# Kernel tuning notes

Hardware: AMD Instinct MI355X
Metric: run time of the kernel (lower is better)

The kernel has to match this reference:

```python
import jax, jax.numpy as jnp
import numpy as np

B, S, HID = 1, 2048, 2048
H, D, R = 16, 256, 64          # heads, head_dim, qk_rope_head_dim
NOPE = D - R
QL, OR, G = 1024, 512, 4       # q_lora_rank, o_lora_rank, o_groups
HPG = H // G
EPS = 1e-6
SCALE = D ** -0.5
STD = 0.02


def setup_inputs() -> dict:
    key = jax.random.key(0)
    ks = jax.random.split(key, 9)
    return {
        "x": jax.random.normal(ks[0], (B, S, HID), jnp.float32),
        "freqs": jax.random.uniform(ks[1], (B, S, R // 2), jnp.float32) * 6.2831853,
        "wq_a": jax.random.normal(ks[2], (QL, HID), jnp.float32) * STD,
        "q_norm_w": jnp.ones((QL,), jnp.float32),
        "wq_b": jax.random.normal(ks[3], (H * D, QL), jnp.float32) * STD,
        "wkv": jax.random.normal(ks[4], (D, HID), jnp.float32) * STD,
        "kv_norm_w": jnp.ones((D,), jnp.float32),
        "wo_a_w": jax.random.normal(ks[5], (G * OR, HPG * D), jnp.float32) * STD,
        "wo_b": jax.random.normal(ks[6], (HID, G * OR), jnp.float32) * STD,
        "attn_sink": jnp.zeros((H,), jnp.float32),
    }


def _rms(x, w):
    return x * jax.lax.rsqrt(jnp.mean(jnp.square(x), -1, keepdims=True) + EPS) * w


def _rot(t, cos, sin, conj=False):
    # t: [..., R]; cos/sin broadcastable to [..., R//2]
    tr = t.reshape(*t.shape[:-1], R // 2, 2)
    x1, x2 = tr[..., 0], tr[..., 1]
    if conj:
        sin = -sin
    out = jnp.stack([x1 * cos - x2 * sin, x1 * sin + x2 * cos], axis=-1)
    return out.reshape(t.shape)


def reference(x, freqs, wq_a, q_norm_w, wq_b, wkv, kv_norm_w, wo_a_w, wo_b, attn_sink):
    cos = jnp.cos(freqs)  # [B,S,R/2]
    sin = jnp.sin(freqs)

    # Q path: LoRA down -> RMSNorm -> up, then per-head RMS rescale (no weight)
    q = _rms(x @ wq_a.T, q_norm_w) @ wq_b.T          # [B,S,H*D]
    q = q.reshape(B, S, H, D)
    q = q * jax.lax.rsqrt(jnp.mean(jnp.square(q), -1, keepdims=True) + EPS)
    q_nope, q_pe = q[..., :NOPE], q[..., NOPE:]

    # shared latent K=V
    kv = _rms(x @ wkv.T, kv_norm_w)                  # [B,S,D]
    kv_nope, kv_pe = kv[..., :NOPE], kv[..., NOPE:]

    # partial RoPE
    q_pe = _rot(q_pe, cos[:, :, None, :], sin[:, :, None, :])
    kv_pe = _rot(kv_pe, cos, sin)

    q = jnp.concatenate([q_nope, q_pe], -1)          # [B,S,H,D]
    kv = jnp.concatenate([kv_nope, kv_pe], -1)       # [B,S,D] shared across heads

    # attention with causal mask + per-head sink column
    scores = jnp.einsum("bshd,btd->bhst", q, kv) * SCALE   # [B,H,S,S]
    mask = jnp.tril(jnp.ones((S, S), bool))
    scores = jnp.where(mask, scores, -jnp.inf)
    sink = jnp.broadcast_to(attn_sink[None, :, None, None], (B, H, S, 1))
    probs = jax.nn.softmax(jnp.concatenate([scores, sink], -1), axis=-1)[..., :-1]
    o = jnp.einsum("bhst,btd->bshd", probs, kv)      # [B,S,H,D]

    # un-rotate the rope part of the output (multiply by conj(freqs_cis))
    o_nope, o_pe = o[..., :NOPE], o[..., NOPE:]
    o_pe = _rot(o_pe, cos[:, :, None, :], sin[:, :, None, :], conj=True)
    o = jnp.concatenate([o_nope, o_pe], -1)

    # grouped (block-diagonal) output LoRA, then up-projection
    o_g = o.reshape(B, S, G, HPG * D)
    w = wo_a_w.reshape(G, OR, HPG * D)
    o_r = jnp.einsum("bsgd,grd->bsgr", o_g, w).reshape(B, S, G * OR)
    return o_r @ wo_b.T                              # [B,S,HID]
```

## Files before the change

kernel.cpp:

```cpp
#include <hip/hip_runtime.h>
#include <hip/hip_bf16.h>

#define S_LEN 2048
#define HID 2048
#define NH 16
#define HD 256
#define NROT 64
#define NOPE 192
#define QL 1024
#define OR_ 512
#define NG 4
#define HPG 4
#define EPS 1e-6f
#define SCALE 0.0625f

typedef __bf16 bf16x8 __attribute__((ext_vector_type(8)));
typedef short s16x8 __attribute__((ext_vector_type(8)));
typedef float f32x4 __attribute__((ext_vector_type(4)));

#define MFMA(a, b, c) __builtin_amdgcn_mfma_f32_16x16x32_bf16( \
    __builtin_bit_cast(bf16x8, a), __builtin_bit_cast(bf16x8, b), c, 0, 0, 0)

__device__ __forceinline__ unsigned short f2bf(float x) {
  unsigned int u = __builtin_bit_cast(unsigned int, x);
  u += 0x7FFFu + ((u >> 16) & 1u);
  return (unsigned short)(u >> 16);
}
__device__ __forceinline__ float bf2f(unsigned short b) {
  unsigned int u = ((unsigned int)b) << 16;
  return __builtin_bit_cast(float, u);
}

#define GLD_LDS16(gp, lp) __builtin_amdgcn_global_load_lds( \
    (__attribute__((address_space(1))) void*)(gp), \
    (__attribute__((address_space(3))) void*)(lp), 16, 0, 0)

__global__ __launch_bounds__(256) void f32_to_bf16(const float* __restrict__ in,
                                                   unsigned short* __restrict__ out, int n4) {
  int i = blockIdx.x * 256 + threadIdx.x;
  if (i < n4) {
    float4 v = ((const float4*)in)[i];
    ushort4 o;
    o.x = f2bf(v.x); o.y = f2bf(v.y); o.z = f2bf(v.z); o.w = f2bf(v.w);
    ((ushort4*)out)[i] = o;
  }
}

__global__ __launch_bounds__(256) void conv5(
    const float* __restrict__ x, const float* __restrict__ wqa,
    const float* __restrict__ wqb, const float* __restrict__ wkv,
    const float* __restrict__ woa,
    unsigned short* __restrict__ xo, unsigned short* __restrict__ wqao,
    unsigned short* __restrict__ wqbo, unsigned short* __restrict__ wkvo,
    unsigned short* __restrict__ woao) {
  int i = blockIdx.x * 256 + threadIdx.x;
  const float* src; unsigned short* dst; int off;
  if (i < 1048576)      { src = x;   dst = xo;   off = i; }
  else if (i < 1572864) { src = wqa; dst = wqao; off = i - 1048576; }
  else if (i < 2621440) { src = wqb; dst = wqbo; off = i - 1572864; }
  else if (i < 2752512) { src = wkv; dst = wkvo; off = i - 2621440; }
  else                  { src = woa; dst = woao; off = i - 2752512; }
  float4 v = ((const float4*)src)[off];
  ushort4 o;
  o.x = f2bf(v.x); o.y = f2bf(v.y); o.z = f2bf(v.z); o.w = f2bf(v.w);
  ((ushort4*)dst)[off] = o;
}

template <int BN>
__global__ __launch_bounds__(256, 2) void gemm_bf16(
    const unsigned short* __restrict__ A, const unsigned short* __restrict__ B,
    void* __restrict__ Cv, int K, int lda, int ldb, int ldc,
    long aoffz, long boffz, long coffz, int store_bf) {
  constexpr int NF = BN / 32;
  __shared__ __align__(16) unsigned short As[128 * 32];
  __shared__ __align__(16) unsigned short Bs[BN * 32];
  A += (size_t)blockIdx.z * aoffz;
  B += (size_t)blockIdx.z * boffz;
  const int tid = threadIdx.x;
  const int wave = tid >> 6, lane = tid & 63;
  const int col = lane & 15, grp = lane >> 4;
  const int wm = wave >> 1, wn = wave & 1;
  const int m0 = blockIdx.y * 128, n0 = blockIdx.x * BN;

  f32x4 acc[4][NF];
#pragma unroll
  for (int i = 0; i < 4; ++i)
#pragma unroll
    for (int j = 0; j < NF; ++j) acc[i][j] = (f32x4){0.f, 0.f, 0.f, 0.f};

  for (int k0 = 0; k0 < K; k0 += 32) {
#pragma unroll
    for (int u = 0; u < 2; ++u) {
      int lin = u * 256 + tid;
      int r = lin >> 2, c8 = (lin & 3) * 8;
      GLD_LDS16(A + (size_t)(m0 + r) * lda + k0 + c8, &As[lin * 8]);
    }
#pragma unroll
    for (int u = 0; u < BN / 64; ++u) {
      int lin = u * 256 + tid;
      int r = lin >> 2, c8 = (lin & 3) * 8;
      GLD_LDS16(B + (size_t)(n0 + r) * ldb + k0 + c8, &Bs[lin * 8]);
    }
    __syncthreads();
    s16x8 a[4], b[NF];
#pragma unroll
    for (int i = 0; i < 4; ++i)
      a[i] = *(const s16x8*)&As[(wm * 64 + i * 16 + col) * 32 + grp * 8];
#pragma unroll
    for (int j = 0; j < NF; ++j)
      b[j] = *(const s16x8*)&Bs[(wn * (BN / 2) + j * 16 + col) * 32 + grp * 8];
#pragma unroll
    for (int i = 0; i < 4; ++i)
#pragma unroll
      for (int j = 0; j < NF; ++j)
        acc[i][j] = MFMA(a[i], b[j], acc[i][j]);
    __syncthreads();
  }

  if (store_bf) {
    unsigned short* C = (unsigned short*)Cv + (size_t)blockIdx.z * coffz;
#pragma unroll
    for (int i = 0; i < 4; ++i)
#pragma unroll
      for (int j = 0; j < NF; ++j)
#pragma unroll
        for (int r = 0; r < 4; ++r)
          C[(size_t)(m0 + wm * 64 + i * 16 + grp * 4 + r) * ldc +
            n0 + wn * (BN / 2) + j * 16 + col] = f2bf(acc[i][j][r]);
  } else {
    float* C = (float*)Cv + (size_t)blockIdx.z * coffz;
#pragma unroll
    for (int i = 0; i < 4; ++i)
#pragma unroll
      for (int j = 0; j < NF; ++j)
#pragma unroll
        for (int r = 0; r < 4; ++r)
          C[(size_t)(m0 + wm * 64 + i * 16 + grp * 4 + r) * ldc +
            n0 + wn * (BN / 2) + j * 16 + col] = acc[i][j][r];
  }
}

__global__ __launch_bounds__(256) void rms_combine2(const float* __restrict__ p,
                                                    unsigned short* __restrict__ out,
                                                    const float* __restrict__ w) {
  int row = blockIdx.x;
  const float* r0 = p + (size_t)row * QL;
  const float* r1 = r0 + 2097152;
  __shared__ float buf[QL];
  __shared__ float red[256];
  float s = 0.f;
  for (int i = threadIdx.x; i < QL; i += 256) {
    float v = r0[i] + r1[i];
    buf[i] = v;
    s += v * v;
  }
  red[threadIdx.x] = s;
  __syncthreads();
  for (int off = 128; off > 0; off >>= 1) {
    if (threadIdx.x < off) red[threadIdx.x] += red[threadIdx.x + off];
    __syncthreads();
  }
  float r = rsqrtf(red[0] / (float)QL + EPS);
  for (int i = threadIdx.x; i < QL; i += 256)
    out[(size_t)row * QL + i] = f2bf(buf[i] * r * w[i]);
}

__global__ __launch_bounds__(256) void kv_combine8(const float* __restrict__ p,
                                                   const float* __restrict__ w,
                                                   const float* __restrict__ freqs,
                                                   unsigned short* __restrict__ kv,
                                                   unsigned short* __restrict__ kvT) {
  int s = blockIdx.x;
  int d = threadIdx.x;
  const float* b = p + (size_t)s * HD + d;
  float v = 0.f;
#pragma unroll
  for (int z = 0; z < 8; ++z) v += b[(size_t)z * 524288];
  __shared__ float red[256];
  __shared__ float sm[256];
  red[d] = v * v;
  __syncthreads();
  for (int off = 128; off > 0; off >>= 1) {
    if (d < off) red[d] += red[d + off];
    __syncthreads();
  }
  float r = rsqrtf(red[0] / 256.0f + EPS);
  float nv = v * r * w[d];
  sm[d] = nv;
  __syncthreads();
  float outv = nv;
  if (d >= NOPE) {
    int j = (d - NOPE) >> 1;
    float f = freqs[(size_t)s * (NROT / 2) + j];
    float c = cosf(f), si = sinf(f);
    float x1 = sm[NOPE + 2 * j], x2 = sm[NOPE + 2 * j + 1];
    outv = ((d & 1) == 0) ? (x1 * c - x2 * si) : (x1 * si + x2 * c);
  }
  unsigned short ov = f2bf(outv);
  kv[(size_t)s * HD + d] = ov;
  kvT[(size_t)(s & ~63) * HD + d * 64 + (s & 63)] = ov;
}

__global__ __launch_bounds__(256, 2) void attn_mfma(
    const unsigned short* __restrict__ qbf,
    const unsigned short* __restrict__ kvbf,
    const unsigned short* __restrict__ kvT,
    const float* __restrict__ sink,
    const float* __restrict__ freqs,
    unsigned short* __restrict__ ob) {
  __shared__ __align__(16) unsigned short kv_s[64 * 264];
  __shared__ __align__(16) unsigned short p_s[64 * 72];
  __shared__ float alpha_s[64];
  __shared__ float inv_s[64];

  const int tid = threadIdx.x;
  const int wave = tid >> 6, lane = tid & 63;
  const int col = lane & 15, grp = lane >> 4;
  const int lin = blockIdx.y * gridDim.x + blockIdx.x;
  const int half = lin >> 8, li = lin & 255;
  const int tr = li & 31;
  const int h = (half == 0) ? (li >> 5) : 8 + (li >> 5);
  const int q0 = ((half == 0) ? (31 - tr) : tr) * 64;
  const int qrow = q0 + wave * 16;

  const unsigned short* qbase =
      qbf + (size_t)(qrow + col) * (NH * HD) + (size_t)h * HD + grp * 8;
#define QDECL(ko, nam) s16x8 nam = *(const s16x8*)(qbase + (ko) * 32);
  QDECL(0, qf0) QDECL(1, qf1) QDECL(2, qf2) QDECL(3, qf3)
  QDECL(4, qf4) QDECL(5, qf5) QDECL(6, qf6) QDECL(7, qf7)

  {
    float sq = 0.f;
#define QSQ(qf) { _Pragma("unroll") \
    for (int j = 0; j < 8; ++j) { float v = bf2f((unsigned short)qf[j]); sq += v * v; } }
    QSQ(qf0) QSQ(qf1) QSQ(qf2) QSQ(qf3) QSQ(qf4) QSQ(qf5) QSQ(qf6) QSQ(qf7)
    sq += __shfl_xor(sq, 16);
    sq += __shfl_xor(sq, 32);
    const float qr_ = rsqrtf(sq * (1.0f / 256.0f) + EPS);
#define QSC(qf) { _Pragma("unroll") \
    for (int j = 0; j < 8; ++j) qf[j] = (short)f2bf(bf2f((unsigned short)qf[j]) * qr_); }
    QSC(qf0) QSC(qf1) QSC(qf2) QSC(qf3) QSC(qf4) QSC(qf5)
    const float* fb = freqs + (size_t)(qrow + col) * (NROT / 2);
#define QSR(qf, jb) { _Pragma("unroll") \
    for (int u = 0; u < 4; ++u) { \
      float f = fb[(jb) + grp * 4 + u]; \
      float c = cosf(f), s = sinf(f); \
      float x1 = bf2f((unsigned short)qf[2 * u]) * qr_; \
      float x2 = bf2f((unsigned short)qf[2 * u + 1]) * qr_; \
      qf[2 * u]     = (short)f2bf(x1 * c - x2 * s); \
      qf[2 * u + 1] = (short)f2bf(x1 * s + x2 * c); } }
    QSR(qf6, 0) QSR(qf7, 16)
  }

  const f32x4 z4 = (f32x4){0.f, 0.f, 0.f, 0.f};
  float m0r = -1e30f, m1r = -1e30f, m2r = -1e30f, m3r = -1e30f;
  float lp0 = 0.f, lp1 = 0.f, lp2 = 0.f, lp3 = 0.f;

#define FOR16(M) M(0,0,o00) M(0,1,o01) M(0,2,o02) M(0,3,o03) \
                 M(1,0,o10) M(1,1,o11) M(1,2,o12) M(1,3,o13) \
                 M(2,0,o20) M(2,1,o21) M(2,2,o22) M(2,3,o23) \
                 M(3,0,o30) M(3,1,o31) M(3,2,o32) M(3,3,o33)
#define DECLO(i, j, onam) f32x4 onam = z4;
  FOR16(DECLO)

  const int tS = tid >> 5, ddS = (tid & 31) * 8;

  {
    const unsigned short* sb = kvbf + (size_t)tS * HD + ddS;
#pragma unroll
    for (int k = 0; k < 8; ++k)
      *(s16x8*)&kv_s[(tS + 8 * k) * 264 + ddS] = *(const s16x8*)(sb + (size_t)(8 * k) * HD);
  }

  const int nch = q0 / 64 + 1;
  for (int ch = 0; ch < nch; ++ch) {
    const int t0 = ch * 64;
    __syncthreads();

    const bool havest = (ch + 1 < nch);
    s16x8 st0 = {}, st1 = {}, st2 = {}, st3 = {}, st4 = {}, st5 = {}, st6 = {}, st7 = {};
    if (havest) {
      const unsigned short* sb = kvbf + (size_t)(t0 + 64 + tS) * HD + ddS;
      st0 = *(const s16x8*)(sb);
      st1 = *(const s16x8*)(sb + 8 * HD);
      st2 = *(const s16x8*)(sb + 16 * HD);
      st3 = *(const s16x8*)(sb + 24 * HD);
      st4 = *(const s16x8*)(sb + 32 * HD);
      st5 = *(const s16x8*)(sb + 40 * HD);
      st6 = *(const s16x8*)(sb + 48 * HD);
      st7 = *(const s16x8*)(sb + 56 * HD);
    }
    const unsigned short* vb = kvT + (size_t)t0 * HD + (size_t)(wave * 64 + col) * 64 + grp * 8;
    s16x8 vf00 = *(const s16x8*)(vb);
    s16x8 vf01 = *(const s16x8*)(vb + 32);
    s16x8 vf10 = *(const s16x8*)(vb + 16 * 64);
    s16x8 vf11 = *(const s16x8*)(vb + 16 * 64 + 32);
    s16x8 vf20 = *(const s16x8*)(vb + 32 * 64);
    s16x8 vf21 = *(const s16x8*)(vb + 32 * 64 + 32);
    s16x8 vf30 = *(const s16x8*)(vb + 48 * 64);
    s16x8 vf31 = *(const s16x8*)(vb + 48 * 64 + 32);

    f32x4 sA0 = z4, sA1 = z4, sA2 = z4, sA3 = z4;
    __builtin_amdgcn_s_setprio(1);
#define QKS(ko, qf) { \
      s16x8 b0 = *(const s16x8*)&kv_s[col * 264 + (ko) * 32 + grp * 8]; \
      s16x8 b1 = *(const s16x8*)&kv_s[(16 + col) * 264 + (ko) * 32 + grp * 8]; \
      s16x8 b2 = *(const s16x8*)&kv_s[(32 + col) * 264 + (ko) * 32 + grp * 8]; \
      s16x8 b3 = *(const s16x8*)&kv_s[(48 + col) * 264 + (ko) * 32 + grp * 8]; \
      sA0 = MFMA(qf, b0, sA0); sA1 = MFMA(qf, b1, sA1); \
      sA2 = MFMA(qf, b2, sA2); sA3 = MFMA(qf, b3, sA3); }
    QKS(0, qf0) QKS(1, qf1) QKS(2, qf2) QKS(3, qf3)
    QKS(4, qf4) QKS(5, qf5) QKS(6, qf6) QKS(7, qf7)
    __builtin_amdgcn_s_setprio(0);

#define MASKR(r) { int sg = qrow + grp * 4 + (r); \
    sA0[r] = (t0 + col <= sg)      ? sA0[r] * SCALE : -1e30f; \
    sA1[r] = (t0 + 16 + col <= sg) ? sA1[r] * SCALE : -1e30f; \
    sA2[r] = (t0 + 32 + col <= sg) ? sA2[r] * SCALE : -1e30f; \
    sA3[r] = (t0 + 48 + col <= sg) ? sA3[r] * SCALE : -1e30f; }
    MASKR(0) MASKR(1) MASKR(2) MASKR(3)

    float a0, a1, a2, a3;
#define MAXR(r, mr, ar) { \
    float v = fmaxf(fmaxf(sA0[r], sA1[r]), fmaxf(sA2[r], sA3[r])); \
    v = fmaxf(v, __shfl_xor(v, 1)); v = fmaxf(v, __shfl_xor(v, 2)); \
    v = fmaxf(v, __shfl_xor(v, 4)); v = fmaxf(v, __shfl_xor(v, 8)); \
    float mn = fmaxf(mr, v); ar = __expf(mr - mn); mr = mn; }
    MAXR(0, m0r, a0) MAXR(1, m1r, a1) MAXR(2, m2r, a2) MAXR(3, m3r, a3)

#define PROW(r, mr, lpr, ar) { \
    float p0 = __expf(sA0[r] - mr); float p1 = __expf(sA1[r] - mr); \
    float p2 = __expf(sA2[r] - mr); float p3 = __expf(sA3[r] - mr); \
    lpr = lpr * ar + (p0 + p1) + (p2 + p3); \
    int prow = (wave * 16 + grp * 4 + (r)) * 72; \
    p_s[prow + col] = f2bf(p0);      p_s[prow + 16 + col] = f2bf(p1); \
    p_s[prow + 32 + col] = f2bf(p2); p_s[prow + 48 + col] = f2bf(p3); }
    PROW(0, m0r, lp0, a0) PROW(1, m1r, lp1, a1) PROW(2, m2r, lp2, a2) PROW(3, m3r, lp3, a3)

    if (col == 0) {
      alpha_s[wave * 16 + grp * 4 + 0] = a0;
      alpha_s[wave * 16 + grp * 4 + 1] = a1;
      alpha_s[wave * 16 + grp * 4 + 2] = a2;
      alpha_s[wave * 16 + grp * 4 + 3] = a3;
    }
    __syncthreads();

    if (havest) {
      *(s16x8*)&kv_s[tS * 264 + ddS]        = st0;
      *(s16x8*)&kv_s[(tS + 8) * 264 + ddS]  = st1;
      *(s16x8*)&kv_s[(tS + 16) * 264 + ddS] = st2;
      *(s16x8*)&kv_s[(tS + 24) * 264 + ddS] = st3;
      *(s16x8*)&kv_s[(tS + 32) * 264 + ddS] = st4;
      *(s16x8*)&kv_s[(tS + 40) * 264 + ddS] = st5;
      *(s16x8*)&kv_s[(tS + 48) * 264 + ddS] = st6;
      *(s16x8*)&kv_s[(tS + 56) * 264 + ddS] = st7;
    }

#define RESC(i) { f32x4 av = (f32x4){alpha_s[(i)*16 + grp*4 + 0], alpha_s[(i)*16 + grp*4 + 1], \
                                     alpha_s[(i)*16 + grp*4 + 2], alpha_s[(i)*16 + grp*4 + 3]}; \
    o##i##0 *= av; o##i##1 *= av; o##i##2 *= av; o##i##3 *= av; }
    RESC(0) RESC(1) RESC(2) RESC(3)

    s16x8 pf00 = *(const s16x8*)&p_s[(0 * 16 + col) * 72 + grp * 8];
    s16x8 pf01 = *(const s16x8*)&p_s[(0 * 16 + col) * 72 + 32 + grp * 8];
    s16x8 pf10 = *(const s16x8*)&p_s[(1 * 16 + col) * 72 + grp * 8];
    s16x8 pf11 = *(const s16x8*)&p_s[(1 * 16 + col) * 72 + 32 + grp * 8];
    s16x8 pf20 = *(const s16x8*)&p_s[(2 * 16 + col) * 72 + grp * 8];
    s16x8 pf21 = *(const s16x8*)&p_s[(2 * 16 + col) * 72 + 32 + grp * 8];
    s16x8 pf30 = *(const s16x8*)&p_s[(3 * 16 + col) * 72 + grp * 8];
    s16x8 pf31 = *(const s16x8*)&p_s[(3 * 16 + col) * 72 + 32 + grp * 8];
    __builtin_amdgcn_s_setprio(1);
#define PVJ(j) { \
      o0##j = MFMA(pf00, vf##j##0, o0##j); o0##j = MFMA(pf01, vf##j##1, o0##j); \
      o1##j = MFMA(pf10, vf##j##0, o1##j); o1##j = MFMA(pf11, vf##j##1, o1##j); \
      o2##j = MFMA(pf20, vf##j##0, o2##j); o2##j = MFMA(pf21, vf##j##1, o2##j); \
      o3##j = MFMA(pf30, vf##j##0, o3##j); o3##j = MFMA(pf31, vf##j##1, o3##j); }
    PVJ(0) PVJ(1) PVJ(2) PVJ(3)
    __builtin_amdgcn_s_setprio(0);
  }

  const float sk = sink[h];
  {
#define LRED(lpr) { lpr += __shfl_xor(lpr, 1); lpr += __shfl_xor(lpr, 2); \
                    lpr += __shfl_xor(lpr, 4); lpr += __shfl_xor(lpr, 8); }
    LRED(lp0) LRED(lp1) LRED(lp2) LRED(lp3)
    float i0 = 1.f / (lp0 + __expf(sk - m0r));
    float i1 = 1.f / (lp1 + __expf(sk - m1r));
    float i2 = 1.f / (lp2 + __expf(sk - m2r));
    float i3 = 1.f / (lp3 + __expf(sk - m3r));
    if (col == 0) {
      inv_s[wave * 16 + grp * 4 + 0] = i0;
      inv_s[wave * 16 + grp * 4 + 1] = i1;
      inv_s[wave * 16 + grp * 4 + 2] = i2;
      inv_s[wave * 16 + grp * 4 + 3] = i3;
    }
  }
  __syncthreads();

#define EPIJ(i, j, onam, ivv) { \
    float v0 = onam[0] * ivv[0]; float v1 = onam[1] * ivv[1]; \
    float v2 = onam[2] * ivv[2]; float v3 = onam[3] * ivv[3]; \
    if (wave == 3) { \
      int jr = ((j) * 16 + col) >> 1; \
      float f0 = freqs[(size_t)(q0 + (i) * 16 + grp * 4 + 0) * 32 + jr]; \
      float f1 = freqs[(size_t)(q0 + (i) * 16 + grp * 4 + 1) * 32 + jr]; \
      float f2 = freqs[(size_t)(q0 + (i) * 16 + grp * 4 + 2) * 32 + jr]; \
      float f3 = freqs[(size_t)(q0 + (i) * 16 + grp * 4 + 3) * 32 + jr]; \
      float p0 = __shfl_xor(v0, 1), p1 = __shfl_xor(v1, 1); \
      float p2 = __shfl_xor(v2, 1), p3 = __shfl_xor(v3, 1); \
      v0 = (col & 1) ? (v0 * cosf(f0) - p0 * sinf(f0)) : (v0 * cosf(f0) + p0 * sinf(f0)); \
      v1 = (col & 1) ? (v1 * cosf(f1) - p1 * sinf(f1)) : (v1 * cosf(f1) + p1 * sinf(f1)); \
      v2 = (col & 1) ? (v2 * cosf(f2) - p2 * sinf(f2)) : (v2 * cosf(f2) + p2 * sinf(f2)); \
      v3 = (col & 1) ? (v3 * cosf(f3) - p3 * sinf(f3)) : (v3 * cosf(f3) + p3 * sinf(f3)); \
    } \
    size_t obase = (size_t)(q0 + (i) * 16 + grp * 4) * (NH * HD) + (size_t)h * HD + \
                   wave * 64 + (j) * 16 + col; \
    ob[obase] = f2bf(v0); ob[obase + (NH * HD)] = f2bf(v1); \
    ob[obase + 2 * (NH * HD)] = f2bf(v2); ob[obase + 3 * (NH * HD)] = f2bf(v3); }
#define EPII(i) { \
    f32x4 ivv = (f32x4){inv_s[(i)*16 + grp*4 + 0], inv_s[(i)*16 + grp*4 + 1], \
                        inv_s[(i)*16 + grp*4 + 2], inv_s[(i)*16 + grp*4 + 3]}; \
    EPIJ(i, 0, o##i##0, ivv) EPIJ(i, 1, o##i##1, ivv) \
    EPIJ(i, 2, o##i##2, ivv) EPIJ(i, 3, o##i##3, ivv) }
  EPII(0) EPII(1) EPII(2) EPII(3)
}

extern "C" void kernel_launch(void* const* d_in, const int* in_sizes, int n_in,
                              void* d_out, int out_size, void* d_ws, size_t ws_size,
                              hipStream_t stream) {
  const float* x         = (const float*)d_in[0];
  const float* freqs     = (const float*)d_in[1];
  const float* wq_a      = (const float*)d_in[2];
  const float* q_norm_w  = (const float*)d_in[3];
  const float* wq_b      = (const float*)d_in[4];
  const float* wkv       = (const float*)d_in[5];
  const float* kv_norm_w = (const float*)d_in[6];
  const float* wo_a_w    = (const float*)d_in[7];
  const float* wo_b      = (const float*)d_in[8];
  const float* sink      = (const float*)d_in[9];
  float* out = (float*)d_out;

  char* ws = (char*)d_ws;
  const size_t MB = 1024 * 1024;
  unsigned short* qa_bf   = (unsigned short*)(ws + 0 * MB);
  float*          qa_p    = (float*)(ws + 4 * MB);
  unsigned short* q_bf    = (unsigned short*)(ws + 4 * MB);
  unsigned short* orb_bf  = (unsigned short*)(ws + 4 * MB);
  unsigned short* wob_bf  = (unsigned short*)(ws + 12 * MB);
  unsigned short* o_bf    = (unsigned short*)(ws + 20 * MB);
  unsigned short* x_bf    = (unsigned short*)(ws + 20 * MB);
  float*          kv_p    = (float*)(ws + 28 * MB);
  unsigned short* wqa_bf  = (unsigned short*)(ws + 36 * MB);
  unsigned short* wqb_bf  = (unsigned short*)(ws + 40 * MB);
  unsigned short* wkv_bf  = (unsigned short*)(ws + 48 * MB);
  unsigned short* woa_bf  = (unsigned short*)(ws + 49 * MB);
  unsigned short* kv_bf   = (unsigned short*)(ws + 53 * MB);
  unsigned short* kvT_bf  = (unsigned short*)(ws + 54 * MB);

  dim3 blk(256);

  conv5<<<dim3(12800), blk, 0, stream>>>(x, wq_a, wq_b, wkv, wo_a_w,
                                         x_bf, wqa_bf, wqb_bf, wkv_bf, woa_bf);

  gemm_bf16<64><<<dim3(QL / 64, S_LEN / 128, 2), blk, 0, stream>>>(
      x_bf, wqa_bf, qa_p, HID / 2, HID, HID, QL,
      (long)(HID / 2), (long)(HID / 2), (long)S_LEN * QL, 0);
  rms_combine2<<<dim3(S_LEN), blk, 0, stream>>>(qa_p, qa_bf, q_norm_w);
  gemm_bf16<128><<<dim3(NH * HD / 128, S_LEN / 128, 1), blk, 0, stream>>>(
      qa_bf, wqb_bf, q_bf, QL, QL, QL, NH * HD, 0, 0, 0, 1);
  gemm_bf16<64><<<dim3(HD / 64, S_LEN / 128, 8), blk, 0, stream>>>(
      x_bf, wkv_bf, kv_p, HID / 8, HID, HID, HD,
      (long)(HID / 8), (long)(HID / 8), (long)S_LEN * HD, 0);
  kv_combine8<<<dim3(S_LEN), blk, 0, stream>>>(kv_p, kv_norm_w, freqs, kv_bf, kvT_bf);
  attn_mfma<<<dim3(S_LEN / 64, NH), blk, 0, stream>>>(q_bf, kv_bf, kvT_bf, sink, freqs, o_bf);
  f32_to_bf16<<<dim3(4096), blk, 0, stream>>>(wo_b, wob_bf, 4 * 1024 * 1024 / 4);
  gemm_bf16<64><<<dim3(OR_ / 64, S_LEN / 128, NG), blk, 0, stream>>>(
      o_bf, woa_bf, orb_bf, HPG * HD, NH * HD, HPG * HD, NG * OR_,
      (long)(HPG * HD), (long)OR_ * (HPG * HD), (long)OR_, 1);
  gemm_bf16<64><<<dim3(HID / 64, S_LEN / 128, 1), blk, 0, stream>>>(
      orb_bf, wob_bf, out, NG * OR_, NG * OR_, NG * OR_, HID, 0, 0, 0, 0);
}
```

Measured before the change: 381.7 us.

## Software-pipeline attention loop: overlap QK of next chunk with PV of previous

Restructures the flash-attention chunk loop so that each iteration runs the QK^T MFMAs for chunk ch while the PV MFMAs consume probabilities from chunk ch-1, using double-buffered P and alpha shared arrays. It adds a prologue and epilogue and moves the V fragment load to lag one chunk. The aim is to interleave softmax and PV work with QK so the matrix units stay busy and the exposed serialization between phases shrinks, at the cost of more shared memory and register pressure.

```diff
diff --git a/kernel.cpp b/kernel.cpp
--- a/kernel.cpp
+++ b/kernel.cpp
@@ -209,8 +209,8 @@
     const float* __restrict__ freqs,
     unsigned short* __restrict__ ob) {
   __shared__ __align__(16) unsigned short kv_s[64 * 264];
-  __shared__ __align__(16) unsigned short p_s[64 * 72];
-  __shared__ float alpha_s[64];
+  __shared__ __align__(16) unsigned short p_s[2][64 * 72];
+  __shared__ float alpha_s[2][64];
   __shared__ float inv_s[64];
 
   const int tid = threadIdx.x;
@@ -265,43 +265,34 @@
 
   const int tS = tid >> 5, ddS = (tid & 31) * 8;
 
-  {
-    const unsigned short* sb = kvbf + (size_t)tS * HD + ddS;
-#pragma unroll
-    for (int k = 0; k < 8; ++k)
-      *(s16x8*)&kv_s[(tS + 8 * k) * 264 + ddS] = *(const s16x8*)(sb + (size_t)(8 * k) * HD);
-  }
-
-  const int nch = q0 / 64 + 1;
-  for (int ch = 0; ch < nch; ++ch) {
-    const int t0 = ch * 64;
-    __syncthreads();
-
-    const bool havest = (ch + 1 < nch);
-    s16x8 st0 = {}, st1 = {}, st2 = {}, st3 = {}, st4 = {}, st5 = {}, st6 = {}, st7 = {};
-    if (havest) {
-      const unsigned short* sb = kvbf + (size_t)(t0 + 64 + tS) * HD + ddS;
-      st0 = *(const s16x8*)(sb);
-      st1 = *(const s16x8*)(sb + 8 * HD);
-      st2 = *(const s16x8*)(sb + 16 * HD);
-      st3 = *(const s16x8*)(sb + 24 * HD);
-      st4 = *(const s16x8*)(sb + 32 * HD);
-      st5 = *(const s16x8*)(sb + 40 * HD);
-      st6 = *(const s16x8*)(sb + 48 * HD);
-      st7 = *(const s16x8*)(sb + 56 * HD);
-    }
-    const unsigned short* vb = kvT + (size_t)t0 * HD + (size_t)(wave * 64 + col) * 64 + grp * 8;
-    s16x8 vf00 = *(const s16x8*)(vb);
-    s16x8 vf01 = *(const s16x8*)(vb + 32);
-    s16x8 vf10 = *(const s16x8*)(vb + 16 * 64);
-    s16x8 vf11 = *(const s16x8*)(vb + 16 * 64 + 32);
-    s16x8 vf20 = *(const s16x8*)(vb + 32 * 64);
-    s16x8 vf21 = *(const s16x8*)(vb + 32 * 64 + 32);
-    s16x8 vf30 = *(const s16x8*)(vb + 48 * 64);
-    s16x8 vf31 = *(const s16x8*)(vb + 48 * 64 + 32);
-
-    f32x4 sA0 = z4, sA1 = z4, sA2 = z4, sA3 = z4;
-    __builtin_amdgcn_s_setprio(1);
+  s16x8 st0, st1, st2, st3, st4, st5, st6, st7;
+  s16x8 vf00, vf01, vf10, vf11, vf20, vf21, vf30, vf31;
+
+#define STLOAD(tnext) { \
+    const unsigned short* sb = kvbf + (size_t)((tnext) + tS) * HD + ddS; \
+    st0 = *(const s16x8*)(sb);           st1 = *(const s16x8*)(sb + 8 * HD); \
+    st2 = *(const s16x8*)(sb + 16 * HD); st3 = *(const s16x8*)(sb + 24 * HD); \
+    st4 = *(const s16x8*)(sb + 32 * HD); st5 = *(const s16x8*)(sb + 40 * HD); \
+    st6 = *(const s16x8*)(sb + 48 * HD); st7 = *(const s16x8*)(sb + 56 * HD); }
+
+#define STCOMMIT { \
+    *(s16x8*)&kv_s[tS * 264 + ddS]        = st0; \
+    *(s16x8*)&kv_s[(tS + 8) * 264 + ddS]  = st1; \
+    *(s16x8*)&kv_s[(tS + 16) * 264 + ddS] = st2; \
+    *(s16x8*)&kv_s[(tS + 24) * 264 + ddS] = st3; \
+    *(s16x8*)&kv_s[(tS + 32) * 264 + ddS] = st4; \
+    *(s16x8*)&kv_s[(tS + 40) * 264 + ddS] = st5; \
+    *(s16x8*)&kv_s[(tS + 48) * 264 + ddS] = st6; \
+    *(s16x8*)&kv_s[(tS + 56) * 264 + ddS] = st7; }
+
+#define VFLOAD(tch) { \
+    const unsigned short* vb = kvT + (size_t)(tch) * HD + \
+                               (size_t)(wave * 64 + col) * 64 + grp * 8; \
+    vf00 = *(const s16x8*)(vb);           vf01 = *(const s16x8*)(vb + 32); \
+    vf10 = *(const s16x8*)(vb + 16 * 64); vf11 = *(const s16x8*)(vb + 16 * 64 + 32); \
+    vf20 = *(const s16x8*)(vb + 32 * 64); vf21 = *(const s16x8*)(vb + 32 * 64 + 32); \
+    vf30 = *(const s16x8*)(vb + 48 * 64); vf31 = *(const s16x8*)(vb + 48 * 64 + 32); }
+
 #define QKS(ko, qf) { \
       s16x8 b0 = *(const s16x8*)&kv_s[col * 264 + (ko) * 32 + grp * 8]; \
       s16x8 b1 = *(const s16x8*)&kv_s[(16 + col) * 264 + (ko) * 32 + grp * 8]; \
@@ -309,74 +300,106 @@
       s16x8 b3 = *(const s16x8*)&kv_s[(48 + col) * 264 + (ko) * 32 + grp * 8]; \
       sA0 = MFMA(qf, b0, sA0); sA1 = MFMA(qf, b1, sA1); \
       sA2 = MFMA(qf, b2, sA2); sA3 = MFMA(qf, b3, sA3); }
-    QKS(0, qf0) QKS(1, qf1) QKS(2, qf2) QKS(3, qf3)
-    QKS(4, qf4) QKS(5, qf5) QKS(6, qf6) QKS(7, qf7)
-    __builtin_amdgcn_s_setprio(0);
-
-#define MASKR(r) { int sg = qrow + grp * 4 + (r); \
-    sA0[r] = (t0 + col <= sg)      ? sA0[r] * SCALE : -1e30f; \
-    sA1[r] = (t0 + 16 + col <= sg) ? sA1[r] * SCALE : -1e30f; \
-    sA2[r] = (t0 + 32 + col <= sg) ? sA2[r] * SCALE : -1e30f; \
-    sA3[r] = (t0 + 48 + col <= sg) ? sA3[r] * SCALE : -1e30f; }
-    MASKR(0) MASKR(1) MASKR(2) MASKR(3)
-
-    float a0, a1, a2, a3;
+#define QKRUN { \
+    __builtin_amdgcn_s_setprio(1); \
+    QKS(0, qf0) QKS(1, qf1) QKS(2, qf2) QKS(3, qf3) \
+    QKS(4, qf4) QKS(5, qf5) QKS(6, qf6) QKS(7, qf7) \
+    __builtin_amdgcn_s_setprio(0); }
+
+#define MASKR(r, t0v) { int sg = qrow + grp * 4 + (r); \
+    sA0[r] = ((t0v) + col <= sg)      ? sA0[r] * SCALE : -1e30f; \
+    sA1[r] = ((t0v) + 16 + col <= sg) ? sA1[r] * SCALE : -1e30f; \
+    sA2[r] = ((t0v) + 32 + col <= sg) ? sA2[r] * SCALE : -1e30f; \
+    sA3[r] = ((t0v) + 48 + col <= sg) ? sA3[r] * SCALE : -1e30f; }
+
 #define MAXR(r, mr, ar) { \
     float v = fmaxf(fmaxf(sA0[r], sA1[r]), fmaxf(sA2[r], sA3[r])); \
     v = fmaxf(v, __shfl_xor(v, 1)); v = fmaxf(v, __shfl_xor(v, 2)); \
     v = fmaxf(v, __shfl_xor(v, 4)); v = fmaxf(v, __shfl_xor(v, 8)); \
     float mn = fmaxf(mr, v); ar = __expf(mr - mn); mr = mn; }
-    MAXR(0, m0r, a0) MAXR(1, m1r, a1) MAXR(2, m2r, a2) MAXR(3, m3r, a3)
-
-#define PROW(r, mr, lpr, ar) { \
+
+#define PROW(r, mr, lpr, ar, psb) { \
     float p0 = __expf(sA0[r] - mr); float p1 = __expf(sA1[r] - mr); \
     float p2 = __expf(sA2[r] - mr); float p3 = __expf(sA3[r] - mr); \
     lpr = lpr * ar + (p0 + p1) + (p2 + p3); \
     int prow = (wave * 16 + grp * 4 + (r)) * 72; \
-    p_s[prow + col] = f2bf(p0);      p_s[prow + 16 + col] = f2bf(p1); \
-    p_s[prow + 32 + col] = f2bf(p2); p_s[prow + 48 + col] = f2bf(p3); }
-    PROW(0, m0r, lp0, a0) PROW(1, m1r, lp1, a1) PROW(2, m2r, lp2, a2) PROW(3, m3r, lp3, a3)
-
-    if (col == 0) {
-      alpha_s[wave * 16 + grp * 4 + 0] = a0;
-      alpha_s[wave * 16 + grp * 4 + 1] = a1;
-      alpha_s[wave * 16 + grp * 4 + 2] = a2;
-      alpha_s[wave * 16 + grp * 4 + 3] = a3;
-    }
-    __syncthreads();
-
-    if (havest) {
-      *(s16x8*)&kv_s[tS * 264 + ddS]        = st0;
-      *(s16x8*)&kv_s[(tS + 8) * 264 + ddS]  = st1;
-      *(s16x8*)&kv_s[(tS + 16) * 264 + ddS] = st2;
-      *(s16x8*)&kv_s[(tS + 24) * 264 + ddS] = st3;
-      *(s16x8*)&kv_s[(tS + 32) * 264 + ddS] = st4;
-      *(s16x8*)&kv_s[(tS + 40) * 264 + ddS] = st5;
-      *(s16x8*)&kv_s[(tS + 48) * 264 + ddS] = st6;
-      *(s16x8*)&kv_s[(tS + 56) * 264 + ddS] = st7;
-    }
-
-#define RESC(i) { f32x4 av = (f32x4){alpha_s[(i)*16 + grp*4 + 0], alpha_s[(i)*16 + grp*4 + 1], \
-                                     alpha_s[(i)*16 + grp*4 + 2], alpha_s[(i)*16 + grp*4 + 3]}; \
+    psb[prow + col] = f2bf(p0);      psb[prow + 16 + col] = f2bf(p1); \
+    psb[prow + 32 + col] = f2bf(p2); psb[prow + 48 + col] = f2bf(p3); }
+
+#define SMAXRUN(t0v, cur) { \
+    unsigned short* psb = &p_s[cur][0]; \
+    MASKR(0, t0v) MASKR(1, t0v) MASKR(2, t0v) MASKR(3, t0v) \
+    float a0, a1, a2, a3; \
+    MAXR(0, m0r, a0) MAXR(1, m1r, a1) MAXR(2, m2r, a2) MAXR(3, m3r, a3) \
+    PROW(0, m0r, lp0, a0, psb) PROW(1, m1r, lp1, a1, psb) \
+    PROW(2, m2r, lp2, a2, psb) PROW(3, m3r, lp3, a3, psb) \
+    if (col == 0) { \
+      alpha_s[cur][wave * 16 + grp * 4 + 0] = a0; \
+      alpha_s[cur][wave * 16 + grp * 4 + 1] = a1; \
+      alpha_s[cur][wave * 16 + grp * 4 + 2] = a2; \
+      alpha_s[cur][wave * 16 + grp * 4 + 3] = a3; \
+    } }
+
+#define RESC(i, asr) { f32x4 av = (f32x4){asr[(i)*16 + grp*4 + 0], asr[(i)*16 + grp*4 + 1], \
+                                          asr[(i)*16 + grp*4 + 2], asr[(i)*16 + grp*4 + 3]}; \
     o##i##0 *= av; o##i##1 *= av; o##i##2 *= av; o##i##3 *= av; }
-    RESC(0) RESC(1) RESC(2) RESC(3)
-
-    s16x8 pf00 = *(const s16x8*)&p_s[(0 * 16 + col) * 72 + grp * 8];
-    s16x8 pf01 = *(const s16x8*)&p_s[(0 * 16 + col) * 72 + 32 + grp * 8];
-    s16x8 pf10 = *(const s16x8*)&p_s[(1 * 16 + col) * 72 + grp * 8];
-    s16x8 pf11 = *(const s16x8*)&p_s[(1 * 16 + col) * 72 + 32 + grp * 8];
-    s16x8 pf20 = *(const s16x8*)&p_s[(2 * 16 + col) * 72 + grp * 8];
-    s16x8 pf21 = *(const s16x8*)&p_s[(2 * 16 + col) * 72 + 32 + grp * 8];
-    s16x8 pf30 = *(const s16x8*)&p_s[(3 * 16 + col) * 72 + grp * 8];
-    s16x8 pf31 = *(const s16x8*)&p_s[(3 * 16 + col) * 72 + 32 + grp * 8];
-    __builtin_amdgcn_s_setprio(1);
 #define PVJ(j) { \
       o0##j = MFMA(pf00, vf##j##0, o0##j); o0##j = MFMA(pf01, vf##j##1, o0##j); \
       o1##j = MFMA(pf10, vf##j##0, o1##j); o1##j = MFMA(pf11, vf##j##1, o1##j); \
       o2##j = MFMA(pf20, vf##j##0, o2##j); o2##j = MFMA(pf21, vf##j##1, o2##j); \
       o3##j = MFMA(pf30, vf##j##0, o3##j); o3##j = MFMA(pf31, vf##j##1, o3##j); }
-    PVJ(0) PVJ(1) PVJ(2) PVJ(3)
-    __builtin_amdgcn_s_setprio(0);
+#define PVRUN(prev) { \
+    const unsigned short* psr = &p_s[prev][0]; \
+    const float* asr = &alpha_s[prev][0]; \
+    s16x8 pf00 = *(const s16x8*)&psr[(0 * 16 + col) * 72 + grp * 8]; \
+    s16x8 pf01 = *(const s16x8*)&psr[(0 * 16 + col) * 72 + 32 + grp * 8]; \
+    s16x8 pf10 = *(const s16x8*)&psr[(1 * 16 + col) * 72 + grp * 8]; \
+    s16x8 pf11 = *(const s16x8*)&psr[(1 * 16 + col) * 72 + 32 + grp * 8]; \
+    s16x8 pf20 = *(const s16x8*)&psr[(2 * 16 + col) * 72 + grp * 8]; \
+    s16x8 pf21 = *(const s16x8*)&psr[(2 * 16 + col) * 72 + 32 + grp * 8]; \
+    s16x8 pf30 = *(const s16x8*)&psr[(3 * 16 + col) * 72 + grp * 8]; \
+    s16x8 pf31 = *(const s16x8*)&psr[(3 * 16 + col) * 72 + 32 + grp * 8]; \
+    RESC(0, asr) RESC(1, asr) RESC(2, asr) RESC(3, asr) \
+    __builtin_amdgcn_s_setprio(1); \
+    PVJ(0) PVJ(1) PVJ(2) PVJ(3) \
+    __builtin_amdgcn_s_setprio(0); }
+
+  {
+    const unsigned short* sb = kvbf + (size_t)tS * HD + ddS;
+#pragma unroll
+    for (int k = 0; k < 8; ++k)
+      *(s16x8*)&kv_s[(tS + 8 * k) * 264 + ddS] = *(const s16x8*)(sb + (size_t)(8 * k) * HD);
+  }
+
+  const int nch = q0 / 64 + 1;
+
+  {
+    __syncthreads();
+    if (nch > 1) STLOAD(64)
+    f32x4 sA0 = z4, sA1 = z4, sA2 = z4, sA3 = z4;
+    QKRUN
+    __syncthreads();
+    if (nch > 1) STCOMMIT
+    SMAXRUN(0, 0)
+  }
+
+  for (int ch = 1; ch < nch; ++ch) {
+    const int t0 = ch * 64;
+    __syncthreads();
+    VFLOAD((ch - 1) * 64)
+    if (ch + 1 < nch) STLOAD(t0 + 64)
+    f32x4 sA0 = z4, sA1 = z4, sA2 = z4, sA3 = z4;
+    QKRUN
+    __syncthreads();
+    PVRUN((ch - 1) & 1)
+    SMAXRUN(t0, ch & 1)
+    if (ch + 1 < nch) STCOMMIT
+  }
+
+  {
+    __syncthreads();
+    VFLOAD((nch - 1) * 64)
+    PVRUN((nch - 1) & 1)
   }
 
   const float sk = sink[h];
```

After: 400.9 us. 1.05x slower.
